# Kernel optimization log

Hardware: AMD Instinct MI355X
Metric: run time of the kernel (lower is better)

Reference implementation:

```python
import jax, jax.numpy as jnp
import numpy as np

B, S, H, NH = 4, 2048, 1024, 16
DK = H // NH

def setup_inputs() -> dict:
    key = jax.random.key(0)
    ks = jax.random.split(key, 8)
    query = jax.random.normal(ks[0], (B, S, H), dtype=jnp.float32)
    key_t = jax.random.normal(ks[1], (B, S, H), dtype=jnp.float32)
    value = jax.random.normal(ks[2], (B, S, H), dtype=jnp.float32)
    mask = jnp.ones((B, S), dtype=jnp.int32)
    # Linear weights (torch convention: y = x @ W.T + b)
    sc = 1.0 / np.sqrt(H)
    Wq = jax.random.uniform(ks[3], (H, H), jnp.float32, -sc, sc)
    Wk = jax.random.uniform(ks[4], (H, H), jnp.float32, -sc, sc)
    Wv = jax.random.uniform(ks[5], (H, H), jnp.float32, -sc, sc)
    Wo = jax.random.uniform(ks[6], (H, H), jnp.float32, -sc, sc)
    bo = jax.random.uniform(ks[7], (H,), jnp.float32, -sc, sc)
    return {"query": query, "key": key_t, "value": value, "mask": mask,
            "Wq": Wq, "Wk": Wk, "Wv": Wv, "Wo": Wo, "bo": bo}

def reference(query, key, value, mask, Wq, Wk, Wv, Wo, bo):
    # project and split heads: (B,S,H) -> (B,NH,S,DK)
    def split_heads(x, W):
        y = x @ W.T
        return y.reshape(B, S, NH, DK).transpose(0, 2, 1, 3)
    q = split_heads(query, Wq)
    k = split_heads(key, Wk)
    v = split_heads(value, Wv)
    scores = jnp.einsum('bhqd,bhkd->bhqk', q, k) / jnp.sqrt(jnp.float32(DK))
    # outer-product padding mask: (B,S)x(B,S) -> (B,1,S,S)
    m = (mask[:, :, None] * mask[:, None, :])[:, None, :, :]
    scores = jnp.where(m == 0, jnp.float32(-1e9), scores)
    p = jax.nn.softmax(scores, axis=-1)  # dropout off (eval mode)
    x = jnp.einsum('bhqk,bhkd->bhqd', p, v)
    x = x.transpose(0, 2, 1, 3).reshape(B, S, H)
    return x @ Wo.T + bo
```

## Files before the change

### kernel.cpp

```cpp
#include <hip/hip_runtime.h>

typedef unsigned short u16;
typedef __bf16 bf16x8 __attribute__((ext_vector_type(8)));
typedef __bf16 bf16x4 __attribute__((ext_vector_type(4)));
typedef float f32x4 __attribute__((ext_vector_type(4)));

#if __has_builtin(__builtin_amdgcn_exp2f)
#define EXP2(x) __builtin_amdgcn_exp2f(x)
#else
#define EXP2(x) exp2f(x)
#endif

template<int V> struct IC { static constexpr int val = V; };

__device__ __forceinline__ u16 f2bf(float f) {
    unsigned u = __float_as_uint(f);
    u += 0x7fffu + ((u >> 16) & 1u);
    return (u16)(u >> 16);
}

__device__ __forceinline__ void gll16(const void* g, void* l) {
    __builtin_amdgcn_global_load_lds(
        (const __attribute__((address_space(1))) void*)g,
        (__attribute__((address_space(3))) void*)l, 16, 0, 0);
}

__device__ __forceinline__ void cvt_body(const float* __restrict__ in,
                                         u16* __restrict__ out, int i) {
    float4 v = reinterpret_cast<const float4*>(in)[i];
    unsigned long long pack =
        (unsigned long long)f2bf(v.x) |
        ((unsigned long long)f2bf(v.y) << 16) |
        ((unsigned long long)f2bf(v.z) << 32) |
        ((unsigned long long)f2bf(v.w) << 48);
    reinterpret_cast<unsigned long long*>(out)[i] = pack;
}

__global__ __launch_bounds__(256) void cvt_bf16_3(const float* __restrict__ a,
                                                  const float* __restrict__ b,
                                                  const float* __restrict__ c,
                                                  u16* __restrict__ oa,
                                                  u16* __restrict__ ob,
                                                  u16* __restrict__ oc, int n4) {
    int i = blockIdx.x * 256 + threadIdx.x;
    if (i < n4)            cvt_body(a, oa, i);
    else if (i < 2 * n4)   cvt_body(b, ob, i - n4);
    else if (i < 3 * n4)   cvt_body(c, oc, i - 2 * n4);
}

__global__ __launch_bounds__(256) void cvt_bf16_w(const float* __restrict__ a,
                                                  const float* __restrict__ b,
                                                  const float* __restrict__ c,
                                                  const float* __restrict__ d,
                                                  u16* __restrict__ oa,
                                                  u16* __restrict__ ob,
                                                  u16* __restrict__ oc,
                                                  u16* __restrict__ od, int n4) {
    int i = blockIdx.x * 256 + threadIdx.x;
    if (i < n4)            cvt_body(a, oa, i);
    else if (i < 2 * n4)   cvt_body(b, ob, i - n4);
    else if (i < 3 * n4)   cvt_body(c, oc, i - 2 * n4);
    else if (i < 4 * n4)   cvt_body(d, od, i - 3 * n4);
}

template<int MODE>
__global__ __launch_bounds__(256) void gemm_bt(const u16* __restrict__ A,
                                               const u16* __restrict__ B,
                                               void* __restrict__ Cv,
                                               const float* __restrict__ bias) {
    constexpr int K = 1024, N = 1024;
    __shared__ __align__(16) u16 As[128 * 64];
    __shared__ __align__(16) u16 Bs[128 * 64];
    const int tid = threadIdx.x;
    const int wv = tid >> 6, lane = tid & 63, g = lane >> 4, li = lane & 15;
    const int row0 = blockIdx.y << 7, col0 = blockIdx.x << 7;
    const int wm = wv >> 1, wn = wv & 1;

    f32x4 acc[4][4] = {};

    for (int k0 = 0; k0 < K; k0 += 64) {
        __syncthreads();
#pragma unroll
        for (int i = 0; i < 4; i++) {
            const int o   = (wv << 12) + (i << 10) + (lane << 4);
            const int row = o >> 7;
            const int cbg = (o & 127) ^ ((row & 7) << 4);
            gll16(A + (size_t)(row0 + row) * K + k0 + (cbg >> 1),
                  (char*)As + (wv << 12) + (i << 10));
        }
#pragma unroll
        for (int i = 0; i < 4; i++) {
            const int o   = (wv << 12) + (i << 10) + (lane << 4);
            const int row = o >> 7;
            const int cbg = (o & 127) ^ ((row & 7) << 4);
            gll16(B + (size_t)(col0 + row) * K + k0 + (cbg >> 1),
                  (char*)Bs + (wv << 12) + (i << 10));
        }
        __syncthreads();

#pragma unroll
        for (int kk = 0; kk < 2; kk++) {
            bf16x8 af[4], bfr[4];
            const int cb = ((kk << 5) + (g << 3)) << 1;
#pragma unroll
            for (int m = 0; m < 4; m++) {
                const int row = (wm << 6) + (m << 4) + li;
                af[m] = *reinterpret_cast<const bf16x8*>(
                    (const char*)As + (row << 7) + (cb ^ ((row & 7) << 4)));
            }
#pragma unroll
            for (int n = 0; n < 4; n++) {
                const int row = (wn << 6) + (n << 4) + li;
                bfr[n] = *reinterpret_cast<const bf16x8*>(
                    (const char*)Bs + (row << 7) + (cb ^ ((row & 7) << 4)));
            }
#pragma unroll
            for (int m = 0; m < 4; m++)
#pragma unroll
                for (int n = 0; n < 4; n++)
                    acc[m][n] = __builtin_amdgcn_mfma_f32_16x16x32_bf16(
                        af[m], bfr[n], acc[m][n], 0, 0, 0);
        }
    }

    if constexpr (MODE == 0 || MODE == 3) {
        constexpr float SC = (MODE == 3) ? 0.180336880f : 1.0f;
        u16* C = (u16*)Cv;
#pragma unroll
        for (int m = 0; m < 4; m++)
#pragma unroll
            for (int n = 0; n < 4; n++)
#pragma unroll
                for (int r = 0; r < 4; r++) {
                    int row = row0 + (wm << 6) + (m << 4) + (g << 2) + r;
                    int col = col0 + (wn << 6) + (n << 4) + li;
                    C[(size_t)row * N + col] = f2bf(acc[m][n][r] * SC);
                }
    } else if constexpr (MODE == 1) {
        float* C = (float*)Cv;
#pragma unroll
        for (int m = 0; m < 4; m++)
#pragma unroll
            for (int n = 0; n < 4; n++)
#pragma unroll
                for (int r = 0; r < 4; r++) {
                    int row = row0 + (wm << 6) + (m << 4) + (g << 2) + r;
                    int col = col0 + (wn << 6) + (n << 4) + li;
                    C[(size_t)row * N + col] = acc[m][n][r] + bias[col];
                }
    } else {
        u16* C = (u16*)Cv;
#pragma unroll
        for (int m = 0; m < 4; m++)
#pragma unroll
            for (int n = 0; n < 4; n++) {
                int srow = row0 + (wm << 6) + (m << 4) + (g << 2);
                int col  = col0 + (wn << 6) + (n << 4) + li;
                int b = srow >> 11, s = srow & 2047;
                int nh = col >> 6, d = col & 63;
                unsigned long long pack =
                    (unsigned long long)f2bf(acc[m][n][0]) |
                    ((unsigned long long)f2bf(acc[m][n][1]) << 16) |
                    ((unsigned long long)f2bf(acc[m][n][2]) << 32) |
                    ((unsigned long long)f2bf(acc[m][n][3]) << 48);
                *reinterpret_cast<unsigned long long*>(
                    C + ((size_t)((b << 4) + nh) * 64 + d) * 2048 + s) = pack;
            }
    }
}

__global__ __launch_bounds__(512) void attn_fwd(const u16* __restrict__ Q,
                                                const u16* __restrict__ Kp,
                                                const u16* __restrict__ Vt,
                                                const int* __restrict__ mask,
                                                u16* __restrict__ O) {
    constexpr int S = 2048, H = 1024;
    __shared__ __align__(16) char lds[49152];
    __shared__ int sm_bad;
    const int tid = threadIdx.x, wv = tid >> 6, lane = tid & 63;
    const int g = lane >> 4, li = lane & 15;
    const int q0 = blockIdx.x << 7, h = blockIdx.y, b = blockIdx.z;
    const char* Qg = (const char*)(Q + (size_t)(b * S + q0) * H + h * 64);
    const char* Kg = (const char*)(Kp + (size_t)b * S * H + h * 64);
    const char* Vg = (const char*)(Vt + (size_t)(b * 16 + h) * 64 * S);

    auto stageKV = [&](int bufOff, int kv2) {
        const int o   = tid << 4;
        const int row = o >> 7;
        const int cbg = (o & 127) ^ ((row & 7) << 4);
        gll16(Kg + (size_t)(kv2 + row) * 2048 + cbg, lds + bufOff + (wv << 10));
        gll16(Vg + (size_t)row * 4096 + kv2 * 2 + cbg, lds + 16384 + bufOff + (wv << 10));
    };

    if (tid == 0) sm_bad = 0;
#pragma unroll
    for (int i = 0; i < 2; i++) {
        const int o   = (tid << 4) + (i << 13);
        const int row = o >> 7;
        const int cbg = (o & 127) ^ ((row & 7) << 4);
        gll16(Qg + (size_t)row * 2048 + cbg, lds + 32768 + (i << 13) + (wv << 10));
    }
    stageKV(0, 0);

    int z = 0;
#pragma unroll
    for (int j = 0; j < 4; j++) z |= (mask[b * S + (tid << 2) + j] == 0);
    __syncthreads();
    if (z) sm_bad = 1;

    int offKV[2][4], offPW[4], offPR[2];
#pragma unroll
    for (int kk = 0; kk < 2; kk++) {
        offPR[kk] = (li << 7) + (((kk << 6) + (g << 4)) ^ ((li & 7) << 4));
#pragma unroll
        for (int n = 0; n < 4; n++)
            offKV[kk][n] = (((n << 4) + li) << 7) +
                           (((kk << 6) + (g << 4)) ^ ((li & 7) << 4));
    }
#pragma unroll
    for (int n = 0; n < 4; n++)
        offPW[n] = (li << 7) + (((n << 5) + (g << 3)) ^ ((li & 7) << 4));

    char* Pb = lds + 32768 + (wv << 11);

    bf16x8 qf[2];
    qf[0] = *reinterpret_cast<const bf16x8*>(Pb + offPR[0]);
    qf[1] = *reinterpret_cast<const bf16x8*>(Pb + offPR[1]);
    __syncthreads();
    const bool bad = (sm_bad != 0);
    const int  mq  = bad ? mask[b * S + q0 + (wv << 4) + li] : 1;

    f32x4 o_[4] = {};
    float l_ = 0.f;

    auto tile = [&](auto BUF, int kv2) {
        constexpr int KOFF = decltype(BUF)::val * 8192;
        constexpr int VOFF = 16384 + decltype(BUF)::val * 8192;
        f32x4 sc[4] = {};
        __builtin_amdgcn_s_setprio(1);
#pragma unroll
        for (int kk = 0; kk < 2; kk++)
#pragma unroll
            for (int n = 0; n < 4; n++) {
                bf16x8 kf = *reinterpret_cast<const bf16x8*>(lds + KOFF + offKV[kk][n]);
                sc[n] = __builtin_amdgcn_mfma_f32_16x16x32_bf16(kf, qf[kk], sc[n], 0, 0, 0);
            }
        __builtin_amdgcn_s_setprio(0);

        if (bad) {
            const unsigned long long kb = __ballot(mask[b * S + kv2 + lane] != 0);
#pragma unroll
            for (int n = 0; n < 4; n++)
#pragma unroll
                for (int r = 0; r < 4; r++) {
                    const int key = (n << 4) + (g << 2) + r;
                    const bool ok = mq && ((kb >> key) & 1ull);
                    sc[n][r] = ok ? sc[n][r] : -1e9f;
                }
        }

        float rs = 0.f;
#pragma unroll
        for (int n = 0; n < 4; n++)
#pragma unroll
            for (int r = 0; r < 4; r++) {
                const float p = EXP2(sc[n][r]);
                sc[n][r] = p;
                rs += p;
            }
        rs += __shfl_xor(rs, 16);
        rs += __shfl_xor(rs, 32);
        l_ += rs;

#pragma unroll
        for (int n = 0; n < 4; n++) {
            bf16x4 pk;
            pk[0] = (__bf16)sc[n][0]; pk[1] = (__bf16)sc[n][1];
            pk[2] = (__bf16)sc[n][2]; pk[3] = (__bf16)sc[n][3];
            *reinterpret_cast<bf16x4*>(Pb + offPW[n]) = pk;
        }

        __builtin_amdgcn_s_setprio(1);
#pragma unroll
        for (int kk = 0; kk < 2; kk++) {
            bf16x8 pf = *reinterpret_cast<const bf16x8*>(Pb + offPR[kk]);
#pragma unroll
            for (int n = 0; n < 4; n++) {
                bf16x8 vf = *reinterpret_cast<const bf16x8*>(lds + VOFF + offKV[kk][n]);
                o_[n] = __builtin_amdgcn_mfma_f32_16x16x32_bf16(pf, vf, o_[n], 0, 0, 0);
            }
        }
        __builtin_amdgcn_s_setprio(0);
    };

    for (int kv = 0; kv < S; kv += 128) {
        stageKV(8192, kv + 64);
        tile(IC<0>{}, kv);
        __syncthreads();
        if (kv + 128 < S) stageKV(0, kv + 128);
        tile(IC<1>{}, kv + 64);
        __syncthreads();
    }

    float linv[4];
#pragma unroll
    for (int r = 0; r < 4; r++) {
        const float lr = __shfl(l_, (lane & 48) + (g << 2) + r);
        linv[r] = lr > 0.f ? 1.f / lr : 0.f;
    }
#pragma unroll
    for (int n = 0; n < 4; n++)
#pragma unroll
        for (int r = 0; r < 4; r++) {
            const int row = q0 + (wv << 4) + (g << 2) + r;
            const int col = (h << 6) + (n << 4) + li;
            O[(size_t)(b * S + row) * H + col] = f2bf(o_[n][r] * linv[r]);
        }
}

extern "C" void kernel_launch(void* const* d_in, const int* in_sizes, int n_in,
                              void* d_out, int out_size, void* d_ws, size_t ws_size,
                              hipStream_t stream) {
    (void)in_sizes; (void)n_in; (void)out_size; (void)ws_size;
    const float* q    = (const float*)d_in[0];
    const float* k    = (const float*)d_in[1];
    const float* v    = (const float*)d_in[2];
    const int*   mask = (const int*)d_in[3];
    const float* Wq   = (const float*)d_in[4];
    const float* Wk   = (const float*)d_in[5];
    const float* Wv   = (const float*)d_in[6];
    const float* Wo   = (const float*)d_in[7];
    const float* bo   = (const float*)d_in[8];

    const size_t NEL = 8192ull * 1024ull;
    u16* ws  = (u16*)d_ws;
    u16* r0  = ws;
    u16* r1  = ws + NEL;
    u16* r2  = ws + 2 * NEL;
    u16* wqb = ws + 3 * NEL;
    u16* wkb = wqb + 1024 * 1024;
    u16* wvb = wkb + 1024 * 1024;
    u16* wob = wvb + 1024 * 1024;
    u16* r4  = wob + 1024 * 1024;

    const int n4 = (int)(NEL / 4);
    const int cvt_blocks = (3 * n4 + 255) / 256;
    cvt_bf16_3<<<dim3(cvt_blocks), dim3(256), 0, stream>>>(q, k, v, r0, r1, r2, n4);
    cvt_bf16_w<<<dim3(4096), dim3(256), 0, stream>>>(Wq, Wk, Wv, Wo,
                                                     wqb, wkb, wvb, wob, 262144);

    dim3 gg(8, 64), bb(256);
    gemm_bt<3><<<gg, bb, 0, stream>>>(r0, wqb, r4, nullptr);
    gemm_bt<0><<<gg, bb, 0, stream>>>(r1, wkb, r0, nullptr);
    gemm_bt<2><<<gg, bb, 0, stream>>>(r2, wvb, r1, nullptr);

    attn_fwd<<<dim3(16, 16, 4), dim3(512), 0, stream>>>(r4, r0, r1, mask, r2);

    gemm_bt<1><<<gg, bb, 0, stream>>>(r2, wob, d_out, bo);
}
```

Measured before the change: 225.9 us.

## Keep P in registers by permuting V k-index, load Q directly, shrink LDS

Removes the per-tile LDS round trip for the probability matrix. The S accumulator layout is reused directly as the PV MFMA A operand, and V fragments are gathered as two 4-element halves so their k ordering matches. Q fragments are loaded straight from global memory into registers instead of being staged through LDS, which cuts LDS to 32KB and adds an occupancy hint of 8 to the launch bounds. The cost is twice as many, narrower LDS reads for V and uncoalesced 16-byte Q loads.

```diff
diff --git a/kernel.cpp b/kernel.cpp
--- a/kernel.cpp
+++ b/kernel.cpp
@@ -169,18 +169,17 @@
     }
 }
 
-__global__ __launch_bounds__(512) void attn_fwd(const u16* __restrict__ Q,
-                                                const u16* __restrict__ Kp,
-                                                const u16* __restrict__ Vt,
-                                                const int* __restrict__ mask,
-                                                u16* __restrict__ O) {
+__global__ __launch_bounds__(512, 8) void attn_fwd(const u16* __restrict__ Q,
+                                                   const u16* __restrict__ Kp,
+                                                   const u16* __restrict__ Vt,
+                                                   const int* __restrict__ mask,
+                                                   u16* __restrict__ O) {
     constexpr int S = 2048, H = 1024;
-    __shared__ __align__(16) char lds[49152];
+    __shared__ __align__(16) char lds[32768];
     __shared__ int sm_bad;
     const int tid = threadIdx.x, wv = tid >> 6, lane = tid & 63;
     const int g = lane >> 4, li = lane & 15;
     const int q0 = blockIdx.x << 7, h = blockIdx.y, b = blockIdx.z;
-    const char* Qg = (const char*)(Q + (size_t)(b * S + q0) * H + h * 64);
     const char* Kg = (const char*)(Kp + (size_t)b * S * H + h * 64);
     const char* Vg = (const char*)(Vt + (size_t)(b * 16 + h) * 64 * S);
 
@@ -193,42 +192,33 @@
     };
 
     if (tid == 0) sm_bad = 0;
-#pragma unroll
-    for (int i = 0; i < 2; i++) {
-        const int o   = (tid << 4) + (i << 13);
-        const int row = o >> 7;
-        const int cbg = (o & 127) ^ ((row & 7) << 4);
-        gll16(Qg + (size_t)row * 2048 + cbg, lds + 32768 + (i << 13) + (wv << 10));
-    }
     stageKV(0, 0);
+
+    bf16x8 qf[2];
+    {
+        const u16* Qrow = Q + (size_t)(b * S + q0 + (wv << 4) + li) * H + h * 64 + (g << 3);
+        qf[0] = *reinterpret_cast<const bf16x8*>(Qrow);
+        qf[1] = *reinterpret_cast<const bf16x8*>(Qrow + 32);
+    }
 
     int z = 0;
 #pragma unroll
     for (int j = 0; j < 4; j++) z |= (mask[b * S + (tid << 2) + j] == 0);
     __syncthreads();
     if (z) sm_bad = 1;
-
-    int offKV[2][4], offPW[4], offPR[2];
-#pragma unroll
-    for (int kk = 0; kk < 2; kk++) {
-        offPR[kk] = (li << 7) + (((kk << 6) + (g << 4)) ^ ((li & 7) << 4));
-#pragma unroll
-        for (int n = 0; n < 4; n++)
-            offKV[kk][n] = (((n << 4) + li) << 7) +
-                           (((kk << 6) + (g << 4)) ^ ((li & 7) << 4));
-    }
-#pragma unroll
-    for (int n = 0; n < 4; n++)
-        offPW[n] = (li << 7) + (((n << 5) + (g << 3)) ^ ((li & 7) << 4));
-
-    char* Pb = lds + 32768 + (wv << 11);
-
-    bf16x8 qf[2];
-    qf[0] = *reinterpret_cast<const bf16x8*>(Pb + offPR[0]);
-    qf[1] = *reinterpret_cast<const bf16x8*>(Pb + offPR[1]);
     __syncthreads();
     const bool bad = (sm_bad != 0);
     const int  mq  = bad ? mask[b * S + q0 + (wv << 4) + li] : 1;
+
+    int offK[2], offV[2][2];
+#pragma unroll
+    for (int kk = 0; kk < 2; kk++) {
+        offK[kk] = (li << 7) + (((kk << 6) + (g << 4)) ^ ((li & 7) << 4));
+#pragma unroll
+        for (int c = 0; c < 2; c++)
+            offV[kk][c] = (li << 7) +
+                          (((kk << 6) + (c << 5) + (g << 3)) ^ ((li & 7) << 4));
+    }
 
     f32x4 o_[4] = {};
     float l_ = 0.f;
@@ -242,7 +232,8 @@
         for (int kk = 0; kk < 2; kk++)
 #pragma unroll
             for (int n = 0; n < 4; n++) {
-                bf16x8 kf = *reinterpret_cast<const bf16x8*>(lds + KOFF + offKV[kk][n]);
+                bf16x8 kf = *reinterpret_cast<const bf16x8*>(
+                    lds + KOFF + offK[kk] + (n << 11));
                 sc[n] = __builtin_amdgcn_mfma_f32_16x16x32_bf16(kf, qf[kk], sc[n], 0, 0, 0);
             }
         __builtin_amdgcn_s_setprio(0);
@@ -272,21 +263,28 @@
         rs += __shfl_xor(rs, 32);
         l_ += rs;
 
-#pragma unroll
-        for (int n = 0; n < 4; n++) {
-            bf16x4 pk;
-            pk[0] = (__bf16)sc[n][0]; pk[1] = (__bf16)sc[n][1];
-            pk[2] = (__bf16)sc[n][2]; pk[3] = (__bf16)sc[n][3];
-            *reinterpret_cast<bf16x4*>(Pb + offPW[n]) = pk;
+        bf16x8 pf0, pf1;
+#pragma unroll
+        for (int j = 0; j < 4; j++) {
+            pf0[j]     = (__bf16)sc[0][j];
+            pf0[4 + j] = (__bf16)sc[1][j];
+            pf1[j]     = (__bf16)sc[2][j];
+            pf1[4 + j] = (__bf16)sc[3][j];
         }
 
         __builtin_amdgcn_s_setprio(1);
 #pragma unroll
         for (int kk = 0; kk < 2; kk++) {
-            bf16x8 pf = *reinterpret_cast<const bf16x8*>(Pb + offPR[kk]);
+            const bf16x8 pf = kk ? pf1 : pf0;
 #pragma unroll
             for (int n = 0; n < 4; n++) {
-                bf16x8 vf = *reinterpret_cast<const bf16x8*>(lds + VOFF + offKV[kk][n]);
+                bf16x4 v0 = *reinterpret_cast<const bf16x4*>(
+                    lds + VOFF + offV[kk][0] + (n << 11));
+                bf16x4 v1 = *reinterpret_cast<const bf16x4*>(
+                    lds + VOFF + offV[kk][1] + (n << 11));
+                bf16x8 vf;
+#pragma unroll
+                for (int j = 0; j < 4; j++) { vf[j] = v0[j]; vf[4 + j] = v1[j]; }
                 o_[n] = __builtin_amdgcn_mfma_f32_16x16x32_bf16(pf, vf, o_[n], 0, 0, 0);
             }
         }
```

Measured after the change: 305.7 us. 1.35x slower.
